# Performance work log

Measured on AMD Instinct MI355X. Metric: run time of the kernel, lower is better.

## Reference

```python
import jax, jax.numpy as jnp
import numpy as np

FEAT = [(200, 200), (100, 100), (50, 50), (25, 25), (13, 13)]
STRIDES = [4, 8, 16, 32, 64]
SIZES = [32, 64, 128, 256, 512]
RATIOS = np.array([0.5, 1.0, 2.0])
NUM_PER_LEVEL = [h * w * 3 for h, w in FEAT]  # [120000,30000,7500,1875,507]
A_TOTAL = sum(NUM_PER_LEVEL)                  # 159882
B = 4
IMG_H = IMG_W = 800.0
PRE_NMS = 1000      # pre_nms_top_n['testing'] (per level)
POST_NMS = 1000     # post_nms_top_n['testing']
NMS_T = 0.7
SCORE_T = 0.0
MIN_SIZE = 0.001
BBOX_CLIP = float(np.log(1000.0 / 16.0))  # torchvision bbox_xform_clip
LVL_OFFSET = 1000.0                       # > max image coord, for batched_nms trick
LVL_FULL = jnp.asarray(np.repeat(np.arange(5), NUM_PER_LEVEL))  # [A_TOTAL]


def _make_anchors():
    out = []
    for (fh, fw), stride, size in zip(FEAT, STRIDES, SIZES):
        ws = np.sqrt(size * size / RATIOS)
        hs = ws * RATIOS
        base = np.stack([-ws / 2, -hs / 2, ws / 2, hs / 2], axis=1)  # [3,4]
        sx = (np.arange(fw) + 0.5) * stride
        sy = (np.arange(fh) + 0.5) * stride
        cy, cx = np.meshgrid(sy, sx, indexing='ij')
        shifts = np.stack([cx, cy, cx, cy], axis=-1).reshape(-1, 1, 4)
        out.append((shifts + base[None]).reshape(-1, 4))
    return np.concatenate(out, 0).astype(np.float32)


def setup_inputs() -> dict:
    key = jax.random.key(0)
    k1, k2 = jax.random.split(key)
    objectness = jax.random.normal(k1, (B, A_TOTAL), jnp.float32)
    pred_bbox_deltas = jax.random.normal(k2, (B, A_TOTAL, 4), jnp.float32) * 0.5
    anchors = jnp.asarray(_make_anchors())  # real FPN anchor grid [A_TOTAL,4]
    return {"objectness": objectness, "pred_bbox_deltas": pred_bbox_deltas, "anchors": anchors}


def _decode(deltas, anchors):
    # torchvision BoxCoder.decode with weights (1,1,1,1)
    wa = anchors[:, 2] - anchors[:, 0]
    ha = anchors[:, 3] - anchors[:, 1]
    cxa = anchors[:, 0] + 0.5 * wa
    cya = anchors[:, 1] + 0.5 * ha
    dx, dy = deltas[..., 0], deltas[..., 1]
    dw = jnp.minimum(deltas[..., 2], BBOX_CLIP)
    dh = jnp.minimum(deltas[..., 3], BBOX_CLIP)
    cx = dx * wa + cxa
    cy = dy * ha + cya
    w = jnp.exp(dw) * wa
    h = jnp.exp(dh) * ha
    return jnp.stack([cx - 0.5 * w, cy - 0.5 * h, cx + 0.5 * w, cy + 0.5 * h], axis=-1)


def _pairwise_iou(b):
    area = (b[:, 2] - b[:, 0]) * (b[:, 3] - b[:, 1])
    lt = jnp.maximum(b[:, None, :2], b[None, :, :2])
    rb = jnp.minimum(b[:, None, 2:], b[None, :, 2:])
    wh = jnp.clip(rb - lt, 0.0)
    inter = wh[..., 0] * wh[..., 1]
    return inter / (area[:, None] + area[None, :] - inter)


def _nms_image(boxes, scores, lvl):
    # boxes [K,4], scores [K], lvl [K] -> fixed-size [POST_NMS,5] = (x1,y1,x2,y2,score)
    K = boxes.shape[0]
    sg = jax.lax.stop_gradient
    x1 = jnp.clip(boxes[:, 0], 0.0, IMG_W)
    y1 = jnp.clip(boxes[:, 1], 0.0, IMG_H)
    x2 = jnp.clip(boxes[:, 2], 0.0, IMG_W)
    y2 = jnp.clip(boxes[:, 3], 0.0, IMG_H)
    boxes = jnp.stack([x1, y1, x2, y2], axis=1)
    # remove_small_boxes + score threshold
    valid = (sg(x2 - x1) >= MIN_SIZE) & (sg(y2 - y1) >= MIN_SIZE) & (sg(scores) >= SCORE_T)
    order = jnp.argsort(-jnp.where(valid, sg(scores), -jnp.inf))
    boxes = boxes[order]
    scores = scores[order]
    lvl = lvl[order]
    valid = valid[order]
    # batched_nms trick: offset boxes per level so cross-level IoU is 0
    off = sg(boxes) + (lvl.astype(boxes.dtype) * LVL_OFFSET)[:, None]
    iou = _pairwise_iou(off)  # [K,K], decision-only (stop_gradient)
    idx = jnp.arange(K)
    def body(i, keep):
        sup = (iou[i] > NMS_T) & keep[i] & (idx > i)
        return keep & (~sup)
    keep = jax.lax.fori_loop(0, K, body, valid)
    rank = jnp.cumsum(keep) - 1
    sel = keep & (rank < POST_NMS)
    rows = jnp.concatenate([boxes, scores[:, None]], axis=1)
    dst = jnp.where(sel, rank, POST_NMS)  # out-of-range rows dropped
    out = jnp.zeros((POST_NMS, 5), boxes.dtype)
    return out.at[dst].set(jnp.where(sel[:, None], rows, 0.0), mode="drop")


def reference(objectness, pred_bbox_deltas, anchors):
    proposals = _decode(pred_bbox_deltas, anchors)  # [B, A_TOTAL, 4]
    # per-level top-k on objectness logits
    idx_list = []
    off = 0
    for n in NUM_PER_LEVEL:
        k = min(PRE_NMS, n)
        _, ti = jax.lax.top_k(objectness[:, off:off + n], k)
        idx_list.append(ti + off)
        off += n
    top_idx = jnp.concatenate(idx_list, axis=1)  # [B, K=4507]
    obj_k = jnp.take_along_axis(objectness, top_idx, axis=1)
    boxes_k = jnp.take_along_axis(proposals, top_idx[..., None], axis=1)
    lvl_k = LVL_FULL[top_idx]
    scores_k = jax.nn.sigmoid(obj_k)
    # clip + small-box filter + score filter + batched NMS + post-nms topk, per image
    return jax.vmap(_nms_image)(boxes_k, scores_k, lvl_k)  # [B, POST_NMS, 5]
```

## Files before the change

kernel.cpp:

```cpp
#include <hip/hip_runtime.h>
#include <stdint.h>

#define KTOT 4507
#define POSTN 1000
#define ATOT 159882
#define NIMG 4
#define CAND_CAP 4096
#define SLOTCAP 5000
#define BPI 22
#define MT_IMG 73728


__device__ inline unsigned fmono(float f) {
    unsigned u = __float_as_uint(f);
    return (u & 0x80000000u) ? ~u : (u | 0x80000000u);
}
__device__ inline float fmono_inv(unsigned u) {
    unsigned b = (u & 0x80000000u) ? (u ^ 0x80000000u) : ~u;
    return __uint_as_float(b);
}

__device__ inline unsigned long long shfl_u64(unsigned long long v, int src) {
    int lo = __shfl((int)(unsigned)(v & 0xFFFFFFFFULL), src);
    int hi = __shfl((int)(unsigned)(v >> 32), src);
    return ((unsigned long long)(unsigned)hi << 32) | (unsigned)lo;
}

__device__ inline void async16(unsigned long long* lds, const unsigned long long* g) {
#if __has_builtin(__builtin_amdgcn_global_load_lds)
    __builtin_amdgcn_global_load_lds(
        (const __attribute__((address_space(1))) unsigned*)g,
        (__attribute__((address_space(3))) unsigned*)lds, 16, 0, 0);
#else
    *(ulonglong2*)lds = *(const ulonglong2*)g;
#endif
}

__device__ inline int blockExclScan(int v, int* warpSums) {
    int tid = threadIdx.x;
    int lane = tid & 63, wid = tid >> 6;
    int x = v;
#pragma unroll
    for (int d = 1; d < 64; d <<= 1) {
        int y = __shfl_up(x, d);
        if (lane >= d) x += y;
    }
    if (lane == 63) warpSums[wid] = x;
    __syncthreads();
    if (wid == 0) {
        int s = (lane < 16) ? warpSums[lane] : 0;
#pragma unroll
        for (int d = 1; d < 16; d <<= 1) {
            int y = __shfl_up(s, d);
            if (lane >= d) s += y;
        }
        if (lane < 16) warpSums[lane] = s;
    }
    __syncthreads();
    int wpre = (wid == 0) ? 0 : warpSums[wid - 1];
    return wpre + (x - v);
}

__device__ __constant__ int c_lvlOff[5] = {0, 120000, 150000, 157500, 159375};
__device__ __constant__ int c_lvlN[5]   = {120000, 30000, 7500, 1875, 507};
__device__ __constant__ int c_slsz[5]   = {8000, 7500, 7500, 1875, 507};
__device__ __constant__ int c_blvl[BPI] = {0,0,0,0,0,0,0,0,0,0,0,0,0,0,0, 1,1,1,1, 2, 3, 4};
__device__ __constant__ int c_bsl[BPI]  = {0,1,2,3,4,5,6,7,8,9,10,11,12,13,14, 0,1,2,3, 0, 0, 0};
__device__ __constant__ int c_bstart[5] = {0, 15, 19, 20, 21};
__device__ __constant__ int c_bcnt[5]   = {15, 4, 1, 1, 1};

__device__ inline size_t mtBase(int img, int lvl) {
    return (size_t)img * MT_IMG + (lvl < 4 ? (size_t)lvl * 16384 : 65536);
}


__global__ __launch_bounds__(1024) void hist_kernel(const float* __restrict__ obj,
                                                    unsigned* __restrict__ ghist) {
    __shared__ unsigned hist[4096];
    int img = blockIdx.x / BPI, b = blockIdx.x % BPI;
    int lvl = c_blvl[b], sl = c_bsl[b];
    int n = c_lvlN[lvl];
    int s0 = sl * c_slsz[lvl];
    int send = min(s0 + c_slsz[lvl], n);
    const float* src = obj + (size_t)img * ATOT + c_lvlOff[lvl];
    int tid = threadIdx.x;

    for (int i = tid; i < 4096; i += 1024) hist[i] = 0u;
    __syncthreads();

    int base = s0 + tid, last = send - 1;
    float v0 = src[min(base,        last)];
    float v1 = src[min(base + 1024, last)];
    float v2 = src[min(base + 2048, last)];
    float v3 = src[min(base + 3072, last)];
    float v4 = src[min(base + 4096, last)];
    float v5 = src[min(base + 5120, last)];
    float v6 = src[min(base + 6144, last)];
    float v7 = src[min(base + 7168, last)];
#define HIST1(U, VV) if (base + (U)*1024 < send) atomicAdd(&hist[fmono(VV) >> 20], 1u);
    HIST1(0, v0) HIST1(1, v1) HIST1(2, v2) HIST1(3, v3)
    HIST1(4, v4) HIST1(5, v5) HIST1(6, v6) HIST1(7, v7)
#undef HIST1
    __syncthreads();

    unsigned* gh = ghist + (size_t)(img * BPI + b) * 4096;
    for (int i = tid; i < 4096; i += 1024) gh[i] = hist[i];
}


__global__ __launch_bounds__(1024) void gather_kernel(const float* __restrict__ obj,
                                                      const unsigned* __restrict__ ghist,
                                                      unsigned long long* __restrict__ gcand,
                                                      int* __restrict__ gcnt) {
    __shared__ int s_misc[32];
    __shared__ int s_bstar, s_cnt;
    int img = blockIdx.x / BPI, b = blockIdx.x % BPI;
    int lvl = c_blvl[b], sl = c_bsl[b];
    int seg = img * BPI + b;
    int n = c_lvlN[lvl];
    int k = (lvl == 4) ? 507 : 1000;
    int s0 = sl * c_slsz[lvl];
    int send = min(s0 + c_slsz[lvl], n);
    const float* src = obj + (size_t)img * ATOT + c_lvlOff[lvl];
    int tid = threadIdx.x;
    int lane = tid & 63;

    if (tid == 0) s_cnt = 0;

    unsigned hx = 0, hy = 0, hz = 0, hw = 0;
    {
        int bs = c_bstart[lvl], bc = c_bcnt[lvl];
        for (int s = 0; s < bc; s++) {
            const uint4* gh4 = (const uint4*)(ghist + (size_t)(img * BPI + bs + s) * 4096);
            uint4 t = gh4[tid];
            hx += t.x; hy += t.y; hz += t.z; hw += t.w;
        }
    }
    int mysum = (int)(hx + hy + hz + hw);
    int excl = blockExclScan(mysum, s_misc);
    int target = n - k;
    {
        int P = excl;
        if ((int)hx > 0 && P <= target && target < P + (int)hx) s_bstar = 4 * tid + 0;
        P += (int)hx;
        if ((int)hy > 0 && P <= target && target < P + (int)hy) s_bstar = 4 * tid + 1;
        P += (int)hy;
        if ((int)hz > 0 && P <= target && target < P + (int)hz) s_bstar = 4 * tid + 2;
        P += (int)hz;
        if ((int)hw > 0 && P <= target && target < P + (int)hw) s_bstar = 4 * tid + 3;
    }
    __syncthreads();
    int bstar = s_bstar;

    unsigned long long* gc = gcand + (size_t)seg * CAND_CAP;
    int base = s0 + tid, last = send - 1;
    float v0 = src[min(base,        last)];
    float v1 = src[min(base + 1024, last)];
    float v2 = src[min(base + 2048, last)];
    float v3 = src[min(base + 3072, last)];
    float v4 = src[min(base + 4096, last)];
    float v5 = src[min(base + 5120, last)];
    float v6 = src[min(base + 6144, last)];
    float v7 = src[min(base + 7168, last)];
#define PUSH1(U, VV)                                                                     \
    {                                                                                    \
        int ix = base + (U) * 1024;                                                      \
        unsigned key = fmono(VV);                                                        \
        bool s = (ix < send) && ((int)(key >> 20) >= bstar);                             \
        unsigned long long mk = __ballot(s);                                             \
        if (mk) {                                                                        \
            int pre = __popcll(mk & ((1ULL << lane) - 1ULL));                            \
            int ldr = __builtin_ctzll(mk);                                               \
            int basew = 0;                                                               \
            if (lane == ldr) basew = atomicAdd(&s_cnt, __popcll(mk));                    \
            basew = __shfl(basew, ldr);                                                  \
            if (s) {                                                                     \
                int pos = basew + pre;                                                   \
                if (pos < CAND_CAP)                                                      \
                    gc[pos] = ((unsigned long long)key << 32) | (unsigned)(~(unsigned)ix); \
            }                                                                            \
        }                                                                                \
    }
    PUSH1(0, v0) PUSH1(1, v1) PUSH1(2, v2) PUSH1(3, v3)
    PUSH1(4, v4) PUSH1(5, v5) PUSH1(6, v6) PUSH1(7, v7)
#undef PUSH1
    __syncthreads();
    if (tid == 0) gcnt[seg] = min(s_cnt, CAND_CAP);
}


__global__ __launch_bounds__(1024) void rankdecode_kernel(
    const float* __restrict__ deltas, const float* __restrict__ anchors,
    const unsigned long long* __restrict__ gcand, const int* __restrict__ gcnt,
    float* __restrict__ sx1, float* __restrict__ sy1, float* __restrict__ sx2,
    float* __restrict__ sy2, float* __restrict__ sscore,
    float* __restrict__ cx1, float* __restrict__ cy1, float* __restrict__ cx2,
    float* __restrict__ cy2, float* __restrict__ car,
    unsigned long long* __restrict__ ckey, int* __restrict__ cslot, int* __restrict__ cm) {
    __shared__ unsigned long long ck[CAND_CAP];
    __shared__ int s_warp[32];

    int grp = blockIdx.x;
    int img = grp / 5, lvl = grp % 5;
    int kn = (lvl == 4) ? 507 : 1000;
    int koff = lvl * 1000;
    int tid = threadIdx.x;

    int bs = c_bstart[lvl], bc = c_bcnt[lvl];
    int pref = 0;
    for (int s = 0; s < bc; s++) {
        int c = gcnt[img * BPI + bs + s];
        const unsigned long long* segp = gcand + (size_t)(img * BPI + bs + s) * CAND_CAP;
        for (int i = tid; i < c; i += 1024) {
            int d = pref + i;
            if (d < CAND_CAP) ck[d] = segp[i];
        }
        pref += c;
    }
    int m = min(pref, CAND_CAP);
    int P = 512;
    while (P < m) P <<= 1;
    for (int i = m + tid; i < P; i += 1024) ck[i] = 0ULL;
    __syncthreads();

    for (unsigned kk = 2; kk <= (unsigned)P; kk <<= 1) {
        for (unsigned j = kk >> 1; j > 0; j >>= 1) {
            for (unsigned i = (unsigned)tid; i < (unsigned)P; i += 1024) {
                unsigned ixj = i ^ j;
                if (ixj > i) {
                    unsigned long long a = ck[i], b = ck[ixj];
                    bool up = ((i & kk) == 0);
                    if ((a > b) == up) { ck[i] = b; ck[ixj] = a; }
                }
            }
            __syncthreads();
        }
    }

    int r = tid;
    size_t o = (size_t)img * KTOT + koff + r;
    float x1 = 0.f, y1 = 0.f, x2 = 0.f, y2 = 0.f, s = 0.f;
    int valid = 0;
    if (r < kn) {
        unsigned long long key = ck[P - 1 - r];
        int idx = c_lvlOff[lvl] + (int)(~(unsigned)key);
        float logit = fmono_inv((unsigned)(key >> 32));
        float ef = (float)exp(-(double)logit);
        s = 1.0f / __fadd_rn(1.0f, ef);
        float a0 = anchors[(size_t)idx * 4 + 0], a1 = anchors[(size_t)idx * 4 + 1];
        float a2 = anchors[(size_t)idx * 4 + 2], a3 = anchors[(size_t)idx * 4 + 3];
        const float* dp = deltas + ((size_t)img * ATOT + idx) * 4;
        float dx = dp[0], dy = dp[1];
        const float BCLIP = 4.135166556742356f;
        float dw = fminf(dp[2], BCLIP), dh = fminf(dp[3], BCLIP);
        float wa = __fsub_rn(a2, a0), ha = __fsub_rn(a3, a1);
        float cxa = __fadd_rn(a0, __fmul_rn(0.5f, wa));
        float cya = __fadd_rn(a1, __fmul_rn(0.5f, ha));
        float cx = __fadd_rn(__fmul_rn(dx, wa), cxa);
        float cy = __fadd_rn(__fmul_rn(dy, ha), cya);
        float w = __fmul_rn((float)exp((double)dw), wa);
        float h = __fmul_rn((float)exp((double)dh), ha);
        x1 = __fsub_rn(cx, __fmul_rn(0.5f, w));
        y1 = __fsub_rn(cy, __fmul_rn(0.5f, h));
        x2 = __fadd_rn(cx, __fmul_rn(0.5f, w));
        y2 = __fadd_rn(cy, __fmul_rn(0.5f, h));
        x1 = fminf(fmaxf(x1, 0.0f), 800.0f);
        y1 = fminf(fmaxf(y1, 0.0f), 800.0f);
        x2 = fminf(fmaxf(x2, 0.0f), 800.0f);
        y2 = fminf(fmaxf(y2, 0.0f), 800.0f);
        valid = (__fsub_rn(x2, x1) >= 0.001f) && (__fsub_rn(y2, y1) >= 0.001f) && (s >= 0.0f);
        sx1[o] = x1; sy1[o] = y1; sx2[o] = x2; sy2[o] = y2; sscore[o] = s;
    }

    int pos = blockExclScan(valid, s_warp);
    if (valid) {
        float lf = 1000.0f * (float)lvl;
        size_t cb = (size_t)img * SLOTCAP + koff + pos;
        float ox1 = __fadd_rn(x1, lf);
        float oy1 = __fadd_rn(y1, lf);
        float ox2 = __fadd_rn(x2, lf);
        float oy2 = __fadd_rn(y2, lf);
        cx1[cb] = ox1; cy1[cb] = oy1; cx2[cb] = ox2; cy2[cb] = oy2;
        car[cb] = __fmul_rn(__fsub_rn(ox2, ox1), __fsub_rn(oy2, oy1));
        int p = koff + r;
        ckey[cb] = ((unsigned long long)fmono(s) << 32) | (unsigned)(~(unsigned)p);
        cslot[cb] = p;
    }
    if (tid == 1023) cm[grp] = pos + valid;
}


__global__ __launch_bounds__(512) void mask_kernel(
    const float* __restrict__ cx1, const float* __restrict__ cy1,
    const float* __restrict__ cx2, const float* __restrict__ cy2,
    const float* __restrict__ car, const int* __restrict__ cm,
    unsigned long long* __restrict__ maskT) {
    __shared__ float lx1[1000], ly1[1000], lx2[1000], ly2[1000], lar[1000];
    int iq = blockIdx.y;
    int img = iq / 5, lvl = iq % 5;
    int m = cm[iq];
    int W = (m + 63) >> 6;
    int T = (W * (W + 1)) >> 1;
    int tbase = blockIdx.x * 8;
    if (tbase >= T) return;

    size_t cb0 = (size_t)img * SLOTCAP + lvl * 1000;
    for (int q = threadIdx.x; q < m; q += 512) {
        lx1[q] = cx1[cb0 + q]; ly1[q] = cy1[cb0 + q];
        lx2[q] = cx2[cb0 + q]; ly2[q] = cy2[cb0 + q];
        lar[q] = car[cb0 + q];
    }
    __syncthreads();

    int wv = threadIdx.x >> 6, lane = threadIdx.x & 63;
    int t = tbase + wv;
    if (t >= T) return;
    int w = (int)((sqrtf(8.0f * (float)t + 1.0f) - 1.0f) * 0.5f);
    while (((w + 1) * (w + 2)) / 2 <= t) w++;
    while ((w * (w + 1)) / 2 > t) w--;
    int c = t - ((w * (w + 1)) >> 1);

    unsigned long long* MT = maskT + mtBase(img, lvl);

    int j = (w << 6) + lane;
    bool jv = j < m;
    float jx1 = jv ? lx1[j] : 0.f, jy1 = jv ? ly1[j] : 0.f;
    float jx2 = jv ? lx2[j] : 0.f, jy2 = jv ? ly2[j] : 0.f;
    float jar = jv ? lar[j] : 0.f;

    unsigned long long myword = 0ULL;
    int i0 = c << 6, i1 = min(i0 + 64, m);
    for (int i = i0; i < i1; i++) {
        float ix1 = lx1[i], iy1 = ly1[i], ix2 = lx2[i], iy2 = ly2[i], iar = lar[i];
        float ltx = fmaxf(ix1, jx1);
        float lty = fmaxf(iy1, jy1);
        float rbx = fminf(ix2, jx2);
        float rby = fminf(iy2, jy2);
        float wq = fmaxf(__fsub_rn(rbx, ltx), 0.0f);
        float hq = fmaxf(__fsub_rn(rby, lty), 0.0f);
        float inter = __fmul_rn(wq, hq);
        float uni = __fsub_rn(__fadd_rn(iar, jar), inter);
        float iou = inter / uni;
        bool bit = jv && (j > i) && (iou > 0.7f);
        unsigned long long bal = __ballot(bit);
        if (lane == (i & 63)) myword = bal;
    }
    int irow = i0 + lane;
    if (irow < i1) MT[(size_t)irow * 16 + w] = myword;
}


__global__ __launch_bounds__(256, 1) void scan_kernel(
    const unsigned long long* __restrict__ maskT, const int* __restrict__ cm,
    unsigned long long* __restrict__ keepWords) {
    __shared__ unsigned long long M[16384];
    __shared__ unsigned long long s_alive[16], s_kill[16];
    __shared__ int s_go;
    int grp = blockIdx.x;
    int img = grp / 5, lvl = grp % 5;
    int m = cm[grp];
    int tid = threadIdx.x;
    int wv = tid >> 6, lane = tid & 63;
    int w16 = lane & 15, g = lane >> 4;
    int rowgrp = wv * 4 + g;

    if (m == 0) {
        if (tid < 16) keepWords[grp * 16 + tid] = 0ULL;
        return;
    }

    const unsigned long long* src = maskT + mtBase(img, lvl);
    int rounds = (m * 16 + 511) >> 9;
    for (int k = 0; k < rounds; k++) {
        int u = (k << 9) + tid * 2;
        async16(&M[u], &src[u]);
    }
    int fw = m >> 6, tb = m & 63;
    if (tid < 16) {
        unsigned long long a = (tid < fw) ? ~0ULL
                              : (tid == fw && tb) ? ((1ULL << tb) - 1ULL) : 0ULL;
        s_alive[tid] = a;
        s_kill[tid] = 0ULL;
    }
    if (tid == 0) s_go = 1;
    __syncthreads();

    for (int it = 0; it <= m && s_go; it++) {
        unsigned long long p = 0ULL;
        for (int r = rowgrp; r < m; r += 16) {
            unsigned long long aw = s_alive[r >> 6];
            unsigned long long bit = (aw >> (r & 63)) & 1ULL;
            bit &= (unsigned long long)(w16 >= (r >> 6));
            p |= M[r * 16 + w16] & (0ULL - bit);
        }
        p |= shfl_u64(p, (lane + 32) & 63);
        p |= shfl_u64(p, (lane + 16) & 63);
        if (lane < 16 && p) atomicOr(&s_kill[lane], p);
        __syncthreads();
        if (wv == 0) {
            unsigned long long neww = 0ULL, oldw = 0ULL;
            if (lane < 16) {
                unsigned long long initw = (lane < fw) ? ~0ULL
                                          : (lane == fw && tb) ? ((1ULL << tb) - 1ULL) : 0ULL;
                oldw = s_alive[lane];
                neww = initw & ~s_kill[lane];
                s_alive[lane] = neww;
                s_kill[lane] = 0ULL;
            }
            unsigned long long ch = __ballot(lane < 16 && neww != oldw);
            if (lane == 0) s_go = (ch != 0ULL) ? 1 : 0;
        }
        __syncthreads();
    }
    if (tid < 16) keepWords[grp * 16 + tid] = s_alive[tid];
}


__global__ __launch_bounds__(1024) void scanout_kernel(
    const float* __restrict__ sx1, const float* __restrict__ sy1,
    const float* __restrict__ sx2, const float* __restrict__ sy2,
    const float* __restrict__ sscore,
    const unsigned long long* __restrict__ ckey, const int* __restrict__ cslot,
    const int* __restrict__ cm, const unsigned long long* __restrict__ keepWords,
    float* __restrict__ out) {
    __shared__ unsigned long long kkey[SLOTCAP];
    __shared__ int kslot[SLOTCAP];
    __shared__ int s_warp[32];
    __shared__ int s_cnt[5];

    int img = blockIdx.x, tid = threadIdx.x;

    for (int lvl = 0; lvl < 5; lvl++) {
        int m = cm[img * 5 + lvl];
        int koff = lvl * 1000;
        int flag = 0;
        if (tid < m)
            flag = (int)((keepWords[(img * 5 + lvl) * 16 + (tid >> 6)] >> (tid & 63)) & 1ULL);
        int pos = blockExclScan(flag, s_warp);
        if (flag) {
            size_t cb = (size_t)img * SLOTCAP + koff + tid;
            kkey[koff + pos] = ckey[cb];
            kslot[koff + pos] = cslot[cb];
        }
        if (tid == 1023) s_cnt[lvl] = pos + flag;
        __syncthreads();
    }

    int tK = s_cnt[0] + s_cnt[1] + s_cnt[2] + s_cnt[3] + s_cnt[4];

    for (int lvl = 0; lvl < 5; lvl++) {
        int Kc = s_cnt[lvl];
        int koff = lvl * 1000;
        for (int q = tid; q < Kc; q += 1024) {
            unsigned long long key = kkey[koff + q];
            int rank = q;
#pragma unroll
            for (int ol = 0; ol < 5; ol++) {
                if (ol == lvl) continue;
                int lo = 0, hi = s_cnt[ol], base = ol * 1000;
                while (lo < hi) {
                    int mid = (lo + hi) >> 1;
                    if (kkey[base + mid] > key) lo = mid + 1; else hi = mid;
                }
                rank += lo;
            }
            if (rank < POSTN) {
                int slot = kslot[koff + q];
                size_t o = (size_t)img * KTOT + slot;
                float* dst = out + ((size_t)img * POSTN + rank) * 5;
                dst[0] = sx1[o]; dst[1] = sy1[o]; dst[2] = sx2[o]; dst[3] = sy2[o];
                dst[4] = sscore[o];
            }
        }
    }

    int z0 = tK < POSTN ? tK : POSTN;
    int nz = (POSTN - z0) * 5;
    float* ob = out + (size_t)img * POSTN * 5 + (size_t)z0 * 5;
    for (int u = tid; u < nz; u += 1024) ob[u] = 0.f;
}


extern "C" void kernel_launch(void* const* d_in, const int* in_sizes, int n_in,
                              void* d_out, int out_size, void* d_ws, size_t ws_size,
                              hipStream_t stream) {
    const float* obj = (const float*)d_in[0];
    const float* deltas = (const float*)d_in[1];
    const float* anchors = (const float*)d_in[2];
    float* out = (float*)d_out;

    char* ws = (char*)d_ws;
    size_t off = 0;
    auto alloc = [&](size_t bytes) {
        size_t o = off;
        off += (bytes + 255) & ~(size_t)255;
        return o;
    };
    unsigned* ghist = (unsigned*)(ws + alloc((size_t)NIMG * BPI * 4096 * 4));
    int* gcnt = (int*)(ws + alloc((size_t)NIMG * BPI * 4));
    unsigned long long* gcand =
        (unsigned long long*)(ws + alloc((size_t)NIMG * BPI * CAND_CAP * 8));
    float* sx1 = (float*)(ws + alloc((size_t)NIMG * KTOT * 4));
    float* sy1 = (float*)(ws + alloc((size_t)NIMG * KTOT * 4));
    float* sx2 = (float*)(ws + alloc((size_t)NIMG * KTOT * 4));
    float* sy2 = (float*)(ws + alloc((size_t)NIMG * KTOT * 4));
    float* sscore = (float*)(ws + alloc((size_t)NIMG * KTOT * 4));
    float* cx1 = (float*)(ws + alloc((size_t)NIMG * SLOTCAP * 4));
    float* cy1 = (float*)(ws + alloc((size_t)NIMG * SLOTCAP * 4));
    float* cx2 = (float*)(ws + alloc((size_t)NIMG * SLOTCAP * 4));
    float* cy2 = (float*)(ws + alloc((size_t)NIMG * SLOTCAP * 4));
    float* car = (float*)(ws + alloc((size_t)NIMG * SLOTCAP * 4));
    unsigned long long* ckey = (unsigned long long*)(ws + alloc((size_t)NIMG * SLOTCAP * 8));
    int* cslot = (int*)(ws + alloc((size_t)NIMG * SLOTCAP * 4));
    int* cm = (int*)(ws + alloc((size_t)NIMG * 5 * 4));
    unsigned long long* maskT = (unsigned long long*)(ws + alloc((size_t)NIMG * MT_IMG * 8));
    unsigned long long* keepWords = (unsigned long long*)(ws + alloc((size_t)NIMG * 5 * 16 * 8));

    hist_kernel<<<dim3(NIMG * BPI), dim3(1024), 0, stream>>>(obj, ghist);
    gather_kernel<<<dim3(NIMG * BPI), dim3(1024), 0, stream>>>(obj, ghist, gcand, gcnt);
    rankdecode_kernel<<<dim3(NIMG * 5), dim3(1024), 0, stream>>>(
        deltas, anchors, gcand, gcnt, sx1, sy1, sx2, sy2, sscore,
        cx1, cy1, cx2, cy2, car, ckey, cslot, cm);
    mask_kernel<<<dim3(17, NIMG * 5), dim3(512), 0, stream>>>(cx1, cy1, cx2, cy2, car, cm,
                                                              maskT);
    scan_kernel<<<dim3(NIMG * 5), dim3(256), 0, stream>>>(maskT, cm, keepWords);
    scanout_kernel<<<dim3(NIMG), dim3(1024), 0, stream>>>(
        sx1, sy1, sx2, sy2, sscore, ckey, cslot, cm, keepWords, out);
}
```

Before: 176.6 us.

## Hoist threshold bin search into own kernel and prefilter candidates before bitonic sort

Moves the per-level histogram scan that finds the threshold bin into a separate small kernel, so each of the 88 gather blocks no longer re-reduces the level histograms. In rankdecode, when more than 1024 candidates survive, a second 12-bit sub-histogram over the boundary bin finds a finer threshold and compacts the candidates to at most 1024, so the bitonic sort runs on a much smaller power-of-two size. This costs one extra kernel launch and some extra shared-memory atomics and scans, and falls back to the full sort if compaction fails.

```diff
diff --git a/kernel.cpp b/kernel.cpp
--- a/kernel.cpp
+++ b/kernel.cpp
@@ -108,17 +108,50 @@
 }
 
 
+__global__ __launch_bounds__(1024) void bstar_kernel(const unsigned* __restrict__ ghist,
+                                                     int* __restrict__ gbstar) {
+    __shared__ int s_misc[32];
+    __shared__ int s_b;
+    int grp = blockIdx.x;
+    int img = grp / 5, lvl = grp % 5;
+    int n = c_lvlN[lvl];
+    int k = (lvl == 4) ? 507 : 1000;
+    int tid = threadIdx.x;
+
+    unsigned hx = 0, hy = 0, hz = 0, hw = 0;
+    int bs = c_bstart[lvl], bc = c_bcnt[lvl];
+    for (int s = 0; s < bc; s++) {
+        const uint4* gh4 = (const uint4*)(ghist + (size_t)(img * BPI + bs + s) * 4096);
+        uint4 t = gh4[tid];
+        hx += t.x; hy += t.y; hz += t.z; hw += t.w;
+    }
+    int mysum = (int)(hx + hy + hz + hw);
+    int excl = blockExclScan(mysum, s_misc);
+    int target = n - k;
+    {
+        int P = excl;
+        if ((int)hx > 0 && P <= target && target < P + (int)hx) s_b = 4 * tid + 0;
+        P += (int)hx;
+        if ((int)hy > 0 && P <= target && target < P + (int)hy) s_b = 4 * tid + 1;
+        P += (int)hy;
+        if ((int)hz > 0 && P <= target && target < P + (int)hz) s_b = 4 * tid + 2;
+        P += (int)hz;
+        if ((int)hw > 0 && P <= target && target < P + (int)hw) s_b = 4 * tid + 3;
+    }
+    __syncthreads();
+    if (tid == 0) gbstar[grp] = s_b;
+}
+
+
 __global__ __launch_bounds__(1024) void gather_kernel(const float* __restrict__ obj,
-                                                      const unsigned* __restrict__ ghist,
+                                                      const int* __restrict__ gbstar,
                                                       unsigned long long* __restrict__ gcand,
                                                       int* __restrict__ gcnt) {
-    __shared__ int s_misc[32];
-    __shared__ int s_bstar, s_cnt;
+    __shared__ int s_cnt;
     int img = blockIdx.x / BPI, b = blockIdx.x % BPI;
     int lvl = c_blvl[b], sl = c_bsl[b];
     int seg = img * BPI + b;
     int n = c_lvlN[lvl];
-    int k = (lvl == 4) ? 507 : 1000;
     int s0 = sl * c_slsz[lvl];
     int send = min(s0 + c_slsz[lvl], n);
     const float* src = obj + (size_t)img * ATOT + c_lvlOff[lvl];
@@ -126,31 +159,8 @@
     int lane = tid & 63;
 
     if (tid == 0) s_cnt = 0;
-
-    unsigned hx = 0, hy = 0, hz = 0, hw = 0;
-    {
-        int bs = c_bstart[lvl], bc = c_bcnt[lvl];
-        for (int s = 0; s < bc; s++) {
-            const uint4* gh4 = (const uint4*)(ghist + (size_t)(img * BPI + bs + s) * 4096);
-            uint4 t = gh4[tid];
-            hx += t.x; hy += t.y; hz += t.z; hw += t.w;
-        }
-    }
-    int mysum = (int)(hx + hy + hz + hw);
-    int excl = blockExclScan(mysum, s_misc);
-    int target = n - k;
-    {
-        int P = excl;
-        if ((int)hx > 0 && P <= target && target < P + (int)hx) s_bstar = 4 * tid + 0;
-        P += (int)hx;
-        if ((int)hy > 0 && P <= target && target < P + (int)hy) s_bstar = 4 * tid + 1;
-        P += (int)hy;
-        if ((int)hz > 0 && P <= target && target < P + (int)hz) s_bstar = 4 * tid + 2;
-        P += (int)hz;
-        if ((int)hw > 0 && P <= target && target < P + (int)hw) s_bstar = 4 * tid + 3;
-    }
-    __syncthreads();
-    int bstar = s_bstar;
+    int bstar = gbstar[img * 5 + lvl];
+    __syncthreads();
 
     unsigned long long* gc = gcand + (size_t)seg * CAND_CAP;
     int base = s0 + tid, last = send - 1;
@@ -192,13 +202,16 @@
 __global__ __launch_bounds__(1024) void rankdecode_kernel(
     const float* __restrict__ deltas, const float* __restrict__ anchors,
     const unsigned long long* __restrict__ gcand, const int* __restrict__ gcnt,
+    const int* __restrict__ gbstar,
     float* __restrict__ sx1, float* __restrict__ sy1, float* __restrict__ sx2,
     float* __restrict__ sy2, float* __restrict__ sscore,
     float* __restrict__ cx1, float* __restrict__ cy1, float* __restrict__ cx2,
     float* __restrict__ cy2, float* __restrict__ car,
     unsigned long long* __restrict__ ckey, int* __restrict__ cslot, int* __restrict__ cm) {
     __shared__ unsigned long long ck[CAND_CAP];
+    __shared__ __attribute__((aligned(16))) unsigned subh[4096];
     __shared__ int s_warp[32];
+    __shared__ int s_tot, s_sub, s_m2;
 
     int grp = blockIdx.x;
     int img = grp / 5, lvl = grp % 5;
@@ -218,9 +231,71 @@
         pref += c;
     }
     int m = min(pref, CAND_CAP);
+    int bstarv = gbstar[grp];
+    __syncthreads();
+
+    int mm = m;
+    if (m > 1024) {
+        for (int i = tid; i < 4096; i += 1024) subh[i] = 0u;
+        __syncthreads();
+        int c0 = tid, c1 = tid + 1024, c2 = tid + 2048, c3 = tid + 3072;
+        unsigned long long e0 = (c0 < m) ? ck[c0] : 0ULL;
+        unsigned long long e1 = (c1 < m) ? ck[c1] : 0ULL;
+        unsigned long long e2 = (c2 < m) ? ck[c2] : 0ULL;
+        unsigned long long e3 = (c3 < m) ? ck[c3] : 0ULL;
+        int hiCnt = 0;
+#define CLS(E, C)                                                                        \
+        if ((C) < m) {                                                                   \
+            if ((unsigned)((E) >> 52) > (unsigned)bstarv) hiCnt++;                       \
+            else atomicAdd(&subh[(unsigned)(((E) >> 40) & 0xFFFULL)], 1u);               \
+        }
+        CLS(e0, c0) CLS(e1, c1) CLS(e2, c2) CLS(e3, c3)
+#undef CLS
+        int exH = blockExclScan(hiCnt, s_warp);
+        if (tid == 1023) s_tot = exH + hiCnt;
+        __syncthreads();
+        int cntHi = s_tot;
+        int target2 = (m - cntHi) - (kn - cntHi);
+        const uint4* sh4 = (const uint4*)subh;
+        uint4 sc = sh4[tid];
+        int ms2 = (int)(sc.x + sc.y + sc.z + sc.w);
+        int ex2 = blockExclScan(ms2, s_warp);
+        {
+            int Pp = ex2;
+            if ((int)sc.x > 0 && Pp <= target2 && target2 < Pp + (int)sc.x) s_sub = 4 * tid + 0;
+            Pp += (int)sc.x;
+            if ((int)sc.y > 0 && Pp <= target2 && target2 < Pp + (int)sc.y) s_sub = 4 * tid + 1;
+            Pp += (int)sc.y;
+            if ((int)sc.z > 0 && Pp <= target2 && target2 < Pp + (int)sc.z) s_sub = 4 * tid + 2;
+            Pp += (int)sc.z;
+            if ((int)sc.w > 0 && Pp <= target2 && target2 < Pp + (int)sc.w) s_sub = 4 * tid + 3;
+        }
+        __syncthreads();
+        int cstar = s_sub;
+#define FLG(E, C)                                                                        \
+        (((C) < m) && (((unsigned)((E) >> 52) > (unsigned)bstarv) ||                     \
+                       ((unsigned)(((E) >> 40) & 0xFFFULL) >= (unsigned)cstar)))
+        int f0 = FLG(e0, c0), f1 = FLG(e1, c1), f2 = FLG(e2, c2), f3 = FLG(e3, c3);
+#undef FLG
+        int fc = f0 + f1 + f2 + f3;
+        int pos = blockExclScan(fc, s_warp);
+        if (tid == 1023) s_m2 = pos + fc;
+        __syncthreads();
+        int m2 = s_m2;
+        if (m2 <= 1024) {
+            int p = pos;
+            if (f0) ck[p++] = e0;
+            if (f1) ck[p++] = e1;
+            if (f2) ck[p++] = e2;
+            if (f3) ck[p++] = e3;
+            mm = m2;
+        }
+        __syncthreads();
+    }
+
     int P = 512;
-    while (P < m) P <<= 1;
-    for (int i = m + tid; i < P; i += 1024) ck[i] = 0ULL;
+    while (P < mm) P <<= 1;
+    for (int i = mm + tid; i < P; i += 1024) ck[i] = 0ULL;
     __syncthreads();
 
     for (unsigned kk = 2; kk <= (unsigned)P; kk <<= 1) {
@@ -228,9 +303,9 @@
             for (unsigned i = (unsigned)tid; i < (unsigned)P; i += 1024) {
                 unsigned ixj = i ^ j;
                 if (ixj > i) {
-                    unsigned long long a = ck[i], b = ck[ixj];
+                    unsigned long long a = ck[i], b2 = ck[ixj];
                     bool up = ((i & kk) == 0);
-                    if ((a > b) == up) { ck[i] = b; ck[ixj] = a; }
+                    if ((a > b2) == up) { ck[i] = b2; ck[ixj] = a; }
                 }
             }
             __syncthreads();
@@ -498,6 +573,7 @@
     };
     unsigned* ghist = (unsigned*)(ws + alloc((size_t)NIMG * BPI * 4096 * 4));
     int* gcnt = (int*)(ws + alloc((size_t)NIMG * BPI * 4));
+    int* gbstar = (int*)(ws + alloc((size_t)NIMG * 5 * 4));
     unsigned long long* gcand =
         (unsigned long long*)(ws + alloc((size_t)NIMG * BPI * CAND_CAP * 8));
     float* sx1 = (float*)(ws + alloc((size_t)NIMG * KTOT * 4));
@@ -517,9 +593,10 @@
     unsigned long long* keepWords = (unsigned long long*)(ws + alloc((size_t)NIMG * 5 * 16 * 8));
 
     hist_kernel<<<dim3(NIMG * BPI), dim3(1024), 0, stream>>>(obj, ghist);
-    gather_kernel<<<dim3(NIMG * BPI), dim3(1024), 0, stream>>>(obj, ghist, gcand, gcnt);
+    bstar_kernel<<<dim3(NIMG * 5), dim3(1024), 0, stream>>>(ghist, gbstar);
+    gather_kernel<<<dim3(NIMG * BPI), dim3(1024), 0, stream>>>(obj, gbstar, gcand, gcnt);
     rankdecode_kernel<<<dim3(NIMG * 5), dim3(1024), 0, stream>>>(
-        deltas, anchors, gcand, gcnt, sx1, sy1, sx2, sy2, sscore,
+        deltas, anchors, gcand, gcnt, gbstar, sx1, sy1, sx2, sy2, sscore,
         cx1, cy1, cx2, cy2, car, ckey, cslot, cm);
     mask_kernel<<<dim3(17, NIMG * 5), dim3(512), 0, stream>>>(cx1, cy1, cx2, cy2, car, cm,
                                                               maskT);
```

New measurement: 168.9 us. 1.05x faster.
